# Optimization experiments

Hardware: AMD Instinct MI355X
Metric: run time of the kernel (lower is better)

Reference implementation:

```python
import jax, jax.numpy as jnp
import numpy as np

D = 256      # embed_dim
H = 2        # num_heads
DH = D // H  # head_dim = 128
NL = 4       # number of MHA layers
L = 4096     # num faces (queries)
S = 8192     # num edges (keys/values)
E_LOOP = 32  # edges per face loop


def setup_inputs() -> dict:
    key = jax.random.key(0)
    ks = jax.random.split(key, 8)
    v_face_edge_loop = jax.random.randint(ks[0], (L, E_LOOP), 0, S, dtype=jnp.int64)
    v_face_mask = jnp.ones((L,), dtype=bool)
    v_edge_embedding = jax.random.normal(ks[1], (S, D), dtype=jnp.float32)
    v_face_embedding = jax.random.normal(ks[2], (L, D), dtype=jnp.float32)
    # per-layer MHA params, stacked along a leading layer dim (PyTorch layout: W [out,in])
    sc = 1.0 / np.sqrt(D)
    in_proj_w = jax.random.normal(ks[3], (NL, 3 * D, D), dtype=jnp.float32) * sc
    in_proj_b = jnp.zeros((NL, 3 * D), dtype=jnp.float32)
    out_proj_w = jax.random.normal(ks[4], (NL, D, D), dtype=jnp.float32) * sc
    out_proj_b = jnp.zeros((NL, D), dtype=jnp.float32)
    return {
        "v_face_edge_loop": v_face_edge_loop,
        "v_face_mask": v_face_mask,
        "v_edge_embedding": v_edge_embedding,
        "v_face_embedding": v_face_embedding,
        "in_proj_w": in_proj_w,
        "in_proj_b": in_proj_b,
        "out_proj_w": out_proj_w,
        "out_proj_b": out_proj_b,
    }


def _build_mask(loop, face_mask, n_edges):
    # rows with face_mask==False contribute no scatter (mapped to sentinel col S, trimmed)
    rel = jnp.where(face_mask[:, None], loop, -1)
    valid = (rel != -1) & (rel != -2)
    rel = jnp.where(valid, rel, n_edges)  # invalid -> overflow column
    n_faces = loop.shape[0]
    m = jnp.zeros((n_faces, n_edges + 1), dtype=bool)
    m = m.at[jnp.arange(n_faces)[:, None], rel].set(True)
    return m[:, :n_edges]  # [L, S]; True = NOT allowed (PyTorch attn_mask semantics)


def _mha(x, kv, mask, wqkv, bqkv, wo, bo):
    wq, wk, wv = jnp.split(wqkv, 3, axis=0)
    bq, bk, bv = jnp.split(bqkv, 3, axis=0)
    q = (x @ wq.T + bq).reshape(-1, H, DH)    # [L,H,DH]
    k = (kv @ wk.T + bk).reshape(-1, H, DH)   # [S,H,DH]
    v = (kv @ wv.T + bv).reshape(-1, H, DH)   # [S,H,DH]
    scores = jnp.einsum('lhd,shd->hls', q, k) / np.float32(np.sqrt(DH))
    scores = jnp.where(mask[None, :, :], -jnp.inf, scores)
    attn = jax.nn.softmax(scores, axis=-1)
    out = jnp.einsum('hls,shd->lhd', attn, v).reshape(-1, D)
    return out @ wo.T + bo


def reference(v_face_edge_loop, v_face_mask, v_edge_embedding, v_face_embedding,
              in_proj_w, in_proj_b, out_proj_w, out_proj_b):
    n_edges = v_edge_embedding.shape[0]
    mask = _build_mask(v_face_edge_loop, v_face_mask, n_edges)
    x = v_face_embedding
    for i in range(NL):
        x = _mha(x, v_edge_embedding, mask,
                 in_proj_w[i], in_proj_b[i], out_proj_w[i], out_proj_b[i])
    return x
```

## Files before the change

### kernel.cpp

```cpp
#include <hip/hip_runtime.h>
#include <math.h>

typedef _Float16 f16;
typedef _Float16 f16x4 __attribute__((ext_vector_type(4)));
typedef _Float16 f16x8 __attribute__((ext_vector_type(8)));
typedef float f32x4 __attribute__((ext_vector_type(4)));
typedef float f32x16 __attribute__((ext_vector_type(16)));

#define MFMA_F16 __builtin_amdgcn_mfma_f32_16x16x32_f16
#define MFMA32_F16 __builtin_amdgcn_mfma_f32_32x32x16_f16

namespace {
constexpr int kL = 4096;
constexpr int kS = 8192;
constexpr int kD = 256;
constexpr int kH = 2;
constexpr int kDH = 128;
constexpr int kNL = 4;
constexpr int kNS = 8;
constexpr float kScale = 0.08838834764831845f;
}

__global__ __launch_bounds__(256) void cvt_all_k(
    const float* __restrict__ edge, const float* __restrict__ face,
    const float* __restrict__ inw, const float* __restrict__ outw,
    f16* __restrict__ e16, f16* __restrict__ xa,
    f16* __restrict__ win16, f16* __restrict__ wout16) {
  for (int i = blockIdx.x * 256 + threadIdx.x; i < 1048576; i += 1024 * 256) {
    const float* src;
    f16* dst;
    int off;
    if (i < 524288) { src = edge; dst = e16; off = i; }
    else if (i < 786432) { src = face; dst = xa; off = i - 524288; }
    else if (i < 983040) { src = inw; dst = win16; off = i - 786432; }
    else { src = outw; dst = wout16; off = i - 983040; }
    float4 v = *(const float4*)(src + 4 * (size_t)off);
    f16x4 h;
    h[0] = (f16)v.x; h[1] = (f16)v.y; h[2] = (f16)v.z; h[3] = (f16)v.w;
    *(f16x4*)(dst + 4 * (size_t)off) = h;
  }
}

__global__ __launch_bounds__(256) void detect_k(const unsigned int* __restrict__ loopw,
                                                const unsigned char* __restrict__ maskb,
                                                int* __restrict__ flags) {
  __shared__ unsigned int s[3];
  if (threadIdx.x < 3) s[threadIdx.x] = 0;
  __syncthreads();
  unsigned int orodd = 0;
  for (int i = 1 + 2 * threadIdx.x; i < 2048; i += 512) orodd |= loopw[i];
  unsigned int nz1 = 0, nz4 = 0;
  for (int i = threadIdx.x; i < 512; i += 256) {
    unsigned char b = maskb[i];
    if ((i & 3) != 0) nz1 |= b;
    if ((i & 7) == 4) nz4 |= b;
  }
  atomicOr(&s[0], orodd);
  atomicOr(&s[1], nz1);
  atomicOr(&s[2], nz4);
  __syncthreads();
  if (threadIdx.x == 0) {
    flags[0] = (s[0] == 0) ? 2 : 1;
    flags[1] = s[1] ? 1 : (s[2] ? 4 : 8);
  }
}

__device__ __forceinline__ void gemm_core(const f16* __restrict__ A,
                                          const f16* __restrict__ W, int K,
                                          int m0, int n0, int r, int g,
                                          f32x4 acc[2][2]) {
  const f16* ap0 = A + (size_t)(m0 + r) * K + g * 8;
  const f16* ap1 = ap0 + (size_t)16 * K;
  const f16* bp0 = W + (size_t)(n0 + r) * K + g * 8;
  const f16* bp1 = bp0 + (size_t)16 * K;
#pragma unroll 8
  for (int kc = 0; kc < K; kc += 32) {
    f16x8 a0 = *(const f16x8*)(ap0 + kc);
    f16x8 a1 = *(const f16x8*)(ap1 + kc);
    f16x8 b0 = *(const f16x8*)(bp0 + kc);
    f16x8 b1 = *(const f16x8*)(bp1 + kc);
    acc[0][0] = MFMA_F16(a0, b0, acc[0][0], 0, 0, 0);
    acc[0][1] = MFMA_F16(a0, b1, acc[0][1], 0, 0, 0);
    acc[1][0] = MFMA_F16(a1, b0, acc[1][0], 0, 0, 0);
    acc[1][1] = MFMA_F16(a1, b1, acc[1][1], 0, 0, 0);
  }
}

__global__ __launch_bounds__(256) void qkv_gemm_k(
    const f16* __restrict__ x, const f16* __restrict__ e16,
    const f16* __restrict__ wql, const float* __restrict__ biasl,
    f16* __restrict__ q16, f16* __restrict__ k16,
    f16* __restrict__ vt16, f16* __restrict__ v16) {
  const int lane = threadIdx.x & 63;
  const int wid = threadIdx.x >> 6;
  const int r = lane & 15, g = lane >> 4;
  const int bid = blockIdx.x;
  const bool qmode = bid < 256;
  int bx, by;
  const f16* A;
  const f16* W;
  const float* bias;
  if (qmode) {
    bx = bid & 63; by = bid >> 6;
    A = x; W = wql; bias = biasl;
  } else {
    int t = bid - 256;
    bx = t & 127; by = t >> 7;
    A = e16; W = wql + (size_t)kD * kD; bias = biasl + kD;
  }
  const int m0 = bx * 64 + (wid >> 1) * 32;
  const int n0 = by * 64 + (wid & 1) * 32;
  f32x4 acc[2][2] = {};
  gemm_core(A, W, kD, m0, n0, r, g, acc);

#pragma unroll
  for (int mt = 0; mt < 2; ++mt)
#pragma unroll
    for (int nt = 0; nt < 2; ++nt) {
      int col = n0 + nt * 16 + r;
      float bv = bias[col];
#pragma unroll
      for (int i = 0; i < 4; ++i) {
        int row = m0 + mt * 16 + g * 4 + i;
        float v = acc[mt][nt][i] + bv;
        if (qmode) {
          q16[(size_t)row * kD + col] = (f16)v;
        } else if (col < 256) {
          k16[(size_t)row * 256 + col] = (f16)v;
        } else {
          int dv = col - 256;
          vt16[(size_t)dv * kS + row] = (f16)v;
          v16[(size_t)row * 256 + dv] = (f16)v;
        }
      }
    }
}

__global__ __launch_bounds__(256) void gemm_awt_k(
    const f16* __restrict__ A, const f16* __restrict__ W,
    const float* __restrict__ bias, f16* __restrict__ C16,
    float* __restrict__ C32, int M, int N, int K) {
  const int lane = threadIdx.x & 63;
  const int wid = threadIdx.x >> 6;
  const int r = lane & 15, g = lane >> 4;
  const int m0 = blockIdx.x * 64 + (wid >> 1) * 32;
  const int n0 = blockIdx.y * 64 + (wid & 1) * 32;
  f32x4 acc[2][2] = {};
  gemm_core(A, W, K, m0, n0, r, g, acc);
#pragma unroll
  for (int mt = 0; mt < 2; ++mt)
#pragma unroll
    for (int nt = 0; nt < 2; ++nt) {
      int col = n0 + nt * 16 + r;
      float bv = bias[col];
#pragma unroll
      for (int i = 0; i < 4; ++i) {
        int row = m0 + mt * 16 + g * 4 + i;
        float v = acc[mt][nt][i] + bv;
        C16[(size_t)row * N + col] = (f16)v;
        if (C32) C32[(size_t)row * N + col] = v;
      }
    }
}

__device__ __forceinline__ unsigned pkh(float a, float b) {
  auto h2 = __builtin_amdgcn_cvt_pkrtz(a, b);
  return __builtin_bit_cast(unsigned, h2);
}
__device__ __forceinline__ void pswap(unsigned a, unsigned b, unsigned& x,
                                      unsigned& y) {
  typedef int i32x2 __attribute__((ext_vector_type(2)));
  i32x2 rr = __builtin_amdgcn_permlane32_swap((int)a, (int)b, false, false);
  x = (unsigned)rr[0];
  y = (unsigned)rr[1];
}
__device__ __forceinline__ f16x8 build_pfrag(float p0, float p1, float p2,
                                             float p3, float p4, float p5,
                                             float p6, float p7) {
  unsigned a0 = pkh(p0, p1), b0 = pkh(p4, p5);
  unsigned a1 = pkh(p2, p3), b1 = pkh(p6, p7);
  unsigned w0, w1, w2, w3;
  pswap(a0, b0, w0, w2);
  pswap(a1, b1, w1, w3);
  union { unsigned u[4]; f16x8 v; } r;
  r.u[0] = w0; r.u[1] = w1; r.u[2] = w2; r.u[3] = w3;
  return r.v;
}

__global__ __launch_bounds__(256, 2) void attn_dense3_k(
    const f16* __restrict__ Q, const f16* __restrict__ Km,
    const f16* __restrict__ Vt,
    f16* __restrict__ numOut, float* __restrict__ denOut) {
  __shared__ __align__(16) f16 Kl[2][64 * 128];
  __shared__ __align__(16) f16 Vl[2][128 * 64];
  const int tid = threadIdx.x;
  const int lane = tid & 63, wid = tid >> 6;
  const int la = lane & 31, hi = lane >> 5;
  const int h = blockIdx.y;
  const int q0w = blockIdx.x * 128 + wid * 32;
  const int sb0 = blockIdx.z * (kS / kNS);
  const int nt = (kS / kNS) / 64;

  f16x8 qb[8];
#pragma unroll
  for (int kk = 0; kk < 8; ++kk)
    qb[kk] = *(const f16x8*)(Q + (size_t)(q0w + la) * kD + h * kDH + kk * 16 +
                             hi * 8);

  int kSrc[4], kDst[4], vSrc[4], vDst[4];
#pragma unroll
  for (int p = 0; p < 4; ++p) {
    int m = wid * 16 + p * 4 + (lane >> 4);
    int s = lane & 15;
    kSrc[p] = (sb0 + m) * kD + h * kDH + 8 * (s ^ (m & 7));
    kDst[p] = m * 128 + 8 * s;
    int cv = p * 256 + tid;
    int d = cv >> 3, sv = cv & 7;
    vSrc[p] = (h * kDH + d) * kS + sb0 + 8 * (sv ^ (d & 7));
    vDst[p] = d * 64 + 8 * sv;
  }

  f32x16 o0 = {}, o1 = {}, o2 = {}, o3 = {};
  float den = 0.0f;
  f16x8 kst[4], vst[4];

#pragma unroll
  for (int p = 0; p < 4; ++p) {
    kst[p] = *(const f16x8*)(Km + kSrc[p]);
    vst[p] = *(const f16x8*)(Vt + vSrc[p]);
  }
#pragma unroll
  for (int p = 0; p < 4; ++p) {
    *(f16x8*)&Kl[0][kDst[p]] = kst[p];
    *(f16x8*)&Vl[0][vDst[p]] = vst[p];
  }
  __syncthreads();

  for (int t = 0; t < nt; ++t) {
    const int cur = t & 1;
    if (t + 1 < nt) {
#pragma unroll
      for (int p = 0; p < 4; ++p) {
        kst[p] = *(const f16x8*)(Km + kSrc[p] + (t + 1) * 64 * kD);
        vst[p] = *(const f16x8*)(Vt + vSrc[p] + (t + 1) * 64);
      }
    }

    f32x16 st0 = {}, st1 = {};
#pragma unroll
    for (int kk = 0; kk < 8; ++kk) {
      int sl = 8 * ((kk * 2 + hi) ^ (la & 7));
      f16x8 k0 = *(const f16x8*)&Kl[cur][la * 128 + sl];
      f16x8 k1 = *(const f16x8*)&Kl[cur][(32 + la) * 128 + sl];
      st0 = MFMA32_F16(k0, qb[kk], st0, 0, 0, 0);
      st1 = MFMA32_F16(k1, qb[kk], st1, 0, 0, 0);
    }

    f32x16 pe0, pe1;
#pragma unroll
    for (int i = 0; i < 16; ++i) {
      pe0[i] = __expf(st0[i] * kScale);
      pe1[i] = __expf(st1[i] * kScale);
    }
#pragma unroll
    for (int i = 0; i < 16; ++i) den += pe0[i] + pe1[i];

    f16x8 pf[4];
    pf[0] = build_pfrag(pe0[0], pe0[1], pe0[2], pe0[3], pe0[4], pe0[5], pe0[6], pe0[7]);
    pf[1] = build_pfrag(pe0[8], pe0[9], pe0[10], pe0[11], pe0[12], pe0[13], pe0[14], pe0[15]);
    pf[2] = build_pfrag(pe1[0], pe1[1], pe1[2], pe1[3], pe1[4], pe1[5], pe1[6], pe1[7]);
    pf[3] = build_pfrag(pe1[8], pe1[9], pe1[10], pe1[11], pe1[12], pe1[13], pe1[14], pe1[15]);

#pragma unroll
    for (int dt = 0; dt < 4; ++dt) {
      int d = dt * 32 + la;
      f32x16* op = (dt == 0) ? &o0 : (dt == 1) ? &o1 : (dt == 2) ? &o2 : &o3;
#pragma unroll
      for (int ks = 0; ks < 4; ++ks) {
        f16x8 vf = *(const f16x8*)&Vl[cur][d * 64 + 8 * ((ks * 2 + hi) ^ (d & 7))];
        *op = MFMA32_F16(vf, pf[ks], *op, 0, 0, 0);
      }
    }

    if (t + 1 < nt) {
      const int nxt = cur ^ 1;
#pragma unroll
      for (int p = 0; p < 4; ++p) {
        *(f16x8*)&Kl[nxt][kDst[p]] = kst[p];
        *(f16x8*)&Vl[nxt][vDst[p]] = vst[p];
      }
      __syncthreads();
    }
  }

  const size_t base = ((size_t)blockIdx.z * kH + h) * kL + q0w;
#pragma unroll
  for (int dt = 0; dt < 4; ++dt) {
    const f32x16* op = (dt == 0) ? &o0 : (dt == 1) ? &o1 : (dt == 2) ? &o2 : &o3;
#pragma unroll
    for (int gq = 0; gq < 4; ++gq) {
      int d0 = dt * 32 + gq * 8 + 4 * hi;
      f16x4 w;
      w[0] = (f16)(*op)[4 * gq + 0];
      w[1] = (f16)(*op)[4 * gq + 1];
      w[2] = (f16)(*op)[4 * gq + 2];
      w[3] = (f16)(*op)[4 * gq + 3];
      *(f16x4*)&numOut[(base + la) * kDH + d0] = w;
    }
  }
  float dq = den + __shfl_xor(den, 32);
  if (lane < 32) denOut[base + lane] = dq;
}

__global__ __launch_bounds__(256) void corrcomb_k(
    const unsigned int* __restrict__ loopw, const unsigned char* __restrict__ maskb,
    const int* __restrict__ flags,
    const f16* __restrict__ Q, const f16* __restrict__ Km,
    const f16* __restrict__ V,
    const f16* __restrict__ numb, const float* __restrict__ denb,
    f16* __restrict__ out16) {
  __shared__ float cvL[4][128];
  __shared__ float csL[4];
  const int lane = threadIdx.x & 63;
  const int wid = threadIdx.x >> 6;
  const int w = blockIdx.x * 4 + wid;
  const int f = w >> 1, h = w & 1;
  const int lstride = flags[0];
  const int mstride = flags[1];

  int idx = -1, valid = 0;
  if (lane < 32) {
    idx = (int)loopw[(size_t)(f * 32 + lane) * lstride];
    valid = maskb[(size_t)f * mstride] ? 1 : 0;
  }
#pragma unroll
  for (int j = 0; j < 32; ++j) {
    int oidx = __shfl(idx, j);
    if (lane < 32 && j < lane && oidx == idx) valid = 0;
  }

  const size_t qb = (size_t)f * kD + h * kDH + 2 * lane;
  const float qa = (float)Q[qb];
  const float qbv = (float)Q[qb + 1];
  float s0 = 0.0f, cv0 = 0.0f, cv1 = 0.0f;
  for (int e = 0; e < 32; ++e) {
    int ei = __shfl(idx, e);
    int ev = __shfl(valid, e);
    if (!ev) continue;
    size_t kb = (size_t)ei * kD + h * kDH + 2 * lane;
    float part = qa * (float)Km[kb] + qbv * (float)Km[kb + 1];
#pragma unroll
    for (int m = 1; m < 64; m <<= 1) part += __shfl_xor(part, m);
    float pe = __expf(part * kScale);
    s0 += pe;
    cv0 += pe * (float)V[kb];
    cv1 += pe * (float)V[kb + 1];
  }
  cvL[wid][2 * lane] = cv0;
  cvL[wid][2 * lane + 1] = cv1;
  if (lane == 0) csL[wid] = s0;
  __syncthreads();

#pragma unroll
  for (int e = 0; e < 2; ++e) {
    int idx2 = e * 256 + threadIdx.x;
    int floc = idx2 >> 8;
    int c = idx2 & 255;
    int h2 = c >> 7;
    int d = c & 127;
    int widx = floc * 2 + h2;
    int fabs_ = blockIdx.x * 2 + floc;
    float n = -cvL[widx][d];
    float dn = -csL[widx];
#pragma unroll
    for (int z = 0; z < kNS; ++z) {
      n += (float)numb[((size_t)(z * kH + h2) * kL + fabs_) * kDH + d];
      dn += denb[(size_t)(z * kH + h2) * kL + fabs_];
    }
    out16[(size_t)fabs_ * kD + h2 * kDH + d] = (f16)(n / dn);
  }
}

extern "C" void kernel_launch(void* const* d_in, const int* in_sizes, int n_in,
                              void* d_out, int out_size, void* d_ws, size_t ws_size,
                              hipStream_t stream) {
  const unsigned int* loopw = (const unsigned int*)d_in[0];
  const unsigned char* fmask = (const unsigned char*)d_in[1];
  const float* edge = (const float*)d_in[2];
  const float* face = (const float*)d_in[3];
  const float* inw = (const float*)d_in[4];
  const float* inb = (const float*)d_in[5];
  const float* outw = (const float*)d_in[6];
  const float* outb = (const float*)d_in[7];
  float* out = (float*)d_out;

  char* p = (char*)d_ws;
  auto alloc = [&](size_t bytes) {
    char* q = p;
    p += (bytes + 255) & ~(size_t)255;
    return q;
  };
  int* flags = (int*)alloc(256);
  f16* e16 = (f16*)alloc((size_t)kS * kD * 2);
  f16* win16 = (f16*)alloc((size_t)kNL * 3 * kD * kD * 2);
  f16* wout16 = (f16*)alloc((size_t)kNL * kD * kD * 2);
  f16* xa = (f16*)alloc((size_t)kL * kD * 2);
  f16* xb = (f16*)alloc((size_t)kL * kD * 2);
  f16* q16 = (f16*)alloc((size_t)kL * kD * 2);
  f16* k16 = (f16*)alloc((size_t)kS * kD * 2);
  f16* v16 = (f16*)alloc((size_t)kS * kD * 2);
  f16* vt16 = (f16*)alloc((size_t)kS * kD * 2);
  f16* ao16 = (f16*)alloc((size_t)kL * kD * 2);
  f16* numb = (f16*)alloc((size_t)kNS * kH * kL * kDH * 2);
  float* denb = (float*)alloc((size_t)kNS * kH * kL * 4);

  detect_k<<<1, 256, 0, stream>>>(loopw, fmask, flags);
  cvt_all_k<<<1024, 256, 0, stream>>>(edge, face, inw, outw, e16, xa, win16,
                                      wout16);

  f16* x = xa;
  f16* xn = xb;
  for (int l = 0; l < kNL; ++l) {
    const f16* wql = win16 + (size_t)l * 3 * kD * kD;
    qkv_gemm_k<<<1280, 256, 0, stream>>>(x, e16, wql, inb + l * 3 * kD, q16,
                                         k16, vt16, v16);
    attn_dense3_k<<<dim3(kL / 128, kH, kNS), 256, 0, stream>>>(q16, k16, vt16,
                                                               numb, denb);
    corrcomb_k<<<kL / 2, 256, 0, stream>>>(loopw, fmask, flags, q16, k16, v16,
                                           numb, denb, ao16);
    gemm_awt_k<<<dim3(kL / 64, kD / 64), 256, 0, stream>>>(
        ao16, wout16 + (size_t)l * kD * kD, outb + l * kD, xn,
        (l == kNL - 1) ? out : nullptr, kL, kD, kD);
    f16* tmp = x;
    x = xn;
    xn = tmp;
  }
}
```

Before: 434.4 us.

## Transpose V through LDS, flatten attention grid, add setprio, vectorize num stores

The QKV GEMM now stages the V tile in shared memory and writes the transposed Vt with coalesced 16-byte stores instead of scattered 2-byte column writes. The attention kernel uses a 1D grid with head and key-split packed into the low bits so neighbouring blocks share Q tiles. It also raises wave priority around the MFMA sections and packs numerator outputs into f16x8 stores via permlane swaps. Together these aim to cut uncoalesced global writes and improve scheduling, at the cost of extra LDS use and a barrier in the V path.

```diff
diff --git a/kernel.cpp b/kernel.cpp
--- a/kernel.cpp
+++ b/kernel.cpp
@@ -91,6 +91,7 @@
     const f16* __restrict__ wql, const float* __restrict__ biasl,
     f16* __restrict__ q16, f16* __restrict__ k16,
     f16* __restrict__ vt16, f16* __restrict__ v16) {
+  __shared__ __align__(16) f16 Tl[64][72];
   const int lane = threadIdx.x & 63;
   const int wid = threadIdx.x >> 6;
   const int r = lane & 15, g = lane >> 4;
@@ -110,6 +111,7 @@
   }
   const int m0 = bx * 64 + (wid >> 1) * 32;
   const int n0 = by * 64 + (wid & 1) * 32;
+  const bool vmode = !qmode && (by >= 4);
   f32x4 acc[2][2] = {};
   gemm_core(A, W, kD, m0, n0, r, g, acc);
 
@@ -125,15 +127,29 @@
         float v = acc[mt][nt][i] + bv;
         if (qmode) {
           q16[(size_t)row * kD + col] = (f16)v;
-        } else if (col < 256) {
+        } else if (!vmode) {
           k16[(size_t)row * 256 + col] = (f16)v;
         } else {
           int dv = col - 256;
-          vt16[(size_t)dv * kS + row] = (f16)v;
           v16[(size_t)row * 256 + dv] = (f16)v;
+          int nl = (wid & 1) * 32 + nt * 16 + r;
+          int rl = (wid >> 1) * 32 + mt * 16 + g * 4 + i;
+          Tl[nl][rl] = (f16)v;
         }
       }
     }
+  if (vmode) {
+    __syncthreads();
+    const int dvb = (by - 4) * 64;
+    const int key0 = bx * 64;
+#pragma unroll
+    for (int it = 0; it < 2; ++it) {
+      int rowd = it * 32 + (threadIdx.x >> 3);
+      int seg = (threadIdx.x & 7) * 8;
+      *(f16x8*)&vt16[(size_t)(dvb + rowd) * kS + key0 + seg] =
+          *(const f16x8*)&Tl[rowd][seg];
+    }
+  }
 }
 
 __global__ __launch_bounds__(256) void gemm_awt_k(
@@ -187,7 +203,7 @@
   return r.v;
 }
 
-__global__ __launch_bounds__(256, 2) void attn_dense3_k(
+__global__ __launch_bounds__(256, 2) void attn_dense7_k(
     const f16* __restrict__ Q, const f16* __restrict__ Km,
     const f16* __restrict__ Vt,
     f16* __restrict__ numOut, float* __restrict__ denOut) {
@@ -196,9 +212,13 @@
   const int tid = threadIdx.x;
   const int lane = tid & 63, wid = tid >> 6;
   const int la = lane & 31, hi = lane >> 5;
-  const int h = blockIdx.y;
-  const int q0w = blockIdx.x * 128 + wid * 32;
-  const int sb0 = blockIdx.z * (kS / kNS);
+  const int id = blockIdx.x;
+  const int grp = id & 15;
+  const int h = grp & 1;
+  const int z = grp >> 1;
+  const int bx = id >> 4;
+  const int q0w = bx * 128 + wid * 32;
+  const int sb0 = z * (kS / kNS);
   const int nt = (kS / kNS) / 64;
 
   f16x8 qb[8];
@@ -247,6 +267,7 @@
     }
 
     f32x16 st0 = {}, st1 = {};
+    __builtin_amdgcn_s_setprio(1);
 #pragma unroll
     for (int kk = 0; kk < 8; ++kk) {
       int sl = 8 * ((kk * 2 + hi) ^ (la & 7));
@@ -255,6 +276,7 @@
       st0 = MFMA32_F16(k0, qb[kk], st0, 0, 0, 0);
       st1 = MFMA32_F16(k1, qb[kk], st1, 0, 0, 0);
     }
+    __builtin_amdgcn_s_setprio(0);
 
     f32x16 pe0, pe1;
 #pragma unroll
@@ -271,6 +293,7 @@
     pf[2] = build_pfrag(pe1[0], pe1[1], pe1[2], pe1[3], pe1[4], pe1[5], pe1[6], pe1[7]);
     pf[3] = build_pfrag(pe1[8], pe1[9], pe1[10], pe1[11], pe1[12], pe1[13], pe1[14], pe1[15]);
 
+    __builtin_amdgcn_s_setprio(1);
 #pragma unroll
     for (int dt = 0; dt < 4; ++dt) {
       int d = dt * 32 + la;
@@ -281,6 +304,7 @@
         *op = MFMA32_F16(vf, pf[ks], *op, 0, 0, 0);
       }
     }
+    __builtin_amdgcn_s_setprio(0);
 
     if (t + 1 < nt) {
       const int nxt = cur ^ 1;
@@ -293,23 +317,36 @@
     }
   }
 
-  const size_t base = ((size_t)blockIdx.z * kH + h) * kL + q0w;
+  const size_t nbase = ((size_t)z * kH + h) * kL + q0w;
+  const size_t rowb = (nbase + la) * kDH;
 #pragma unroll
   for (int dt = 0; dt < 4; ++dt) {
     const f32x16* op = (dt == 0) ? &o0 : (dt == 1) ? &o1 : (dt == 2) ? &o2 : &o3;
-#pragma unroll
-    for (int gq = 0; gq < 4; ++gq) {
-      int d0 = dt * 32 + gq * 8 + 4 * hi;
-      f16x4 w;
-      w[0] = (f16)(*op)[4 * gq + 0];
-      w[1] = (f16)(*op)[4 * gq + 1];
-      w[2] = (f16)(*op)[4 * gq + 2];
-      w[3] = (f16)(*op)[4 * gq + 3];
-      *(f16x4*)&numOut[(base + la) * kDH + d0] = w;
-    }
+    unsigned u01 = pkh((*op)[0], (*op)[1]);
+    unsigned u23 = pkh((*op)[2], (*op)[3]);
+    unsigned u89 = pkh((*op)[4], (*op)[5]);
+    unsigned uab = pkh((*op)[6], (*op)[7]);
+    unsigned w0, w1, w2, w3;
+    pswap(u01, u89, w0, w2);
+    pswap(u23, uab, w1, w3);
+    union { unsigned u[4]; f16x8 v; } r1;
+    r1.u[0] = w0; r1.u[1] = w1; r1.u[2] = w2; r1.u[3] = w3;
+    *(f16x8*)&numOut[rowb + dt * 32 + hi * 8] = r1.v;
+
+    unsigned v01 = pkh((*op)[8], (*op)[9]);
+    unsigned v23 = pkh((*op)[10], (*op)[11]);
+    unsigned v89 = pkh((*op)[12], (*op)[13]);
+    unsigned vab = pkh((*op)[14], (*op)[15]);
+    unsigned x0, x1, x2, x3;
+    pswap(v01, v89, x0, x2);
+    pswap(v23, vab, x1, x3);
+    union { unsigned u[4]; f16x8 v; } r2;
+    r2.u[0] = x0; r2.u[1] = x1; r2.u[2] = x2; r2.u[3] = x3;
+    *(f16x8*)&numOut[rowb + dt * 32 + 16 + hi * 8] = r2.v;
   }
   float dq = den + __shfl_xor(den, 32);
-  if (lane < 32) denOut[base + lane] = dq;
+  if (lane < 32)
+    denOut[((size_t)z * kH + h) * kL + q0w + lane] = dq;
 }
 
 __global__ __launch_bounds__(256) void corrcomb_k(
@@ -375,7 +412,7 @@
 #pragma unroll
     for (int z = 0; z < kNS; ++z) {
       n += (float)numb[((size_t)(z * kH + h2) * kL + fabs_) * kDH + d];
-      dn += denb[(size_t)(z * kH + h2) * kL + fabs_];
+      dn += denb[((size_t)z * kH + h2) * kL + fabs_];
     }
     out16[(size_t)fabs_ * kD + h2 * kDH + d] = (f16)(n / dn);
   }
@@ -424,8 +461,7 @@
     const f16* wql = win16 + (size_t)l * 3 * kD * kD;
     qkv_gemm_k<<<1280, 256, 0, stream>>>(x, e16, wql, inb + l * 3 * kD, q16,
                                          k16, vt16, v16);
-    attn_dense3_k<<<dim3(kL / 128, kH, kNS), 256, 0, stream>>>(q16, k16, vt16,
-                                                               numb, denb);
+    attn_dense7_k<<<512, 256, 0, stream>>>(q16, k16, vt16, numb, denb);
     corrcomb_k<<<kL / 2, 256, 0, stream>>>(loopw, fmask, flags, q16, k16, v16,
                                            numb, denb, ao16);
     gemm_awt_k<<<dim3(kL / 64, kD / 64), 256, 0, stream>>>(
```

Result: faster. 419.5 us (-3.4%).
